# Kernel optimization log

Measured on AMD Instinct MI355X. Metric: run time of the kernel, lower is better.

## Reference

```python
import jax, jax.numpy as jnp
import numpy as np

KH, KW = 3, 3          # kernel_size
SH, SW = 1, 1          # stride
PH, PW = 1, 1          # padding
NCODEBOOKS = 16
SUBVEC = 36            # (64*3*3)/16
K = 16                 # codewords per codebook (4 tree levels)


def _unfold(x):
    """torch.nn.functional.unfold equivalent: (b,c,h,w) -> (b, c*KH*KW, oh, ow),
    feature dim ordered channel-major (c, ki, kj) like torch."""
    b, c, h, w = x.shape
    xp = jnp.pad(x, ((0, 0), (0, 0), (PH, PH), (PW, PW)))
    oh = (h + 2 * PH - KH) // SH + 1
    ow = (w + 2 * PW - KW) // SW + 1
    patches = [xp[:, :, i:i + (oh - 1) * SH + 1:SH, j:j + (ow - 1) * SW + 1:SW]
               for i in range(KH) for j in range(KW)]
    cols = jnp.stack(patches, axis=2)              # (b, c, KH*KW, oh, ow)
    return cols.reshape(b, c * KH * KW, oh, ow)


def setup_inputs() -> dict:
    key = jax.random.key(0)
    k1, k2, k3, k4, k5 = jax.random.split(key, 5)
    return {
        "x": jax.random.normal(k1, (16, 64, 56, 56), dtype=jnp.float32),
        "split_idxs": jax.random.randint(k2, (NCODEBOOKS, 4), 0, SUBVEC, dtype=jnp.int32),
        "split_vals": jax.random.normal(k3, (NCODEBOOKS, 4, K // 2), dtype=jnp.float32),
        "lookup_tables": jax.random.normal(k4, (NCODEBOOKS, K, 64), dtype=jnp.float32),
        "bias": jax.random.normal(k5, (64,), dtype=jnp.float32),
    }


def reference(x, split_idxs, split_vals, lookup_tables, bias):
    b = x.shape[0]
    cols = _unfold(x)                              # (b, d, oh, ow)
    _, d, oh, ow = cols.shape
    # torch: cols.permute(0,2,1).flatten(0,1) with L=oh*ow row-major
    xf = cols.reshape(b, d, oh * ow).transpose(0, 2, 1).reshape(-1, d)  # (n, d)
    n = xf.shape[0]
    xs = xf.reshape(n, NCODEBOOKS, SUBVEC)
    car = jnp.arange(NCODEBOOKS)
    # Hierarchical 4-level threshold encoding (vectorized over all codebooks):
    # at level t, a point in bucket e compares feature split_idxs[c,t] against
    # split_vals[c,t,e]; new bucket = 2*e + (v >= thr)  (matches the serial
    # bucket-list construction: '<' -> left child, '>=' -> right child).
    enc = jnp.zeros((n, NCODEBOOKS), dtype=jnp.int32)
    for t in range(4):
        v = xs[:, car, split_idxs[:, t]]           # (n, NCODEBOOKS)
        thr = split_vals[car[None, :], t, enc]     # (n, NCODEBOOKS)
        enc = 2 * enc + (v >= thr).astype(jnp.int32)
    # LUT gather-sum (equivalent to one_hot(enc) @ lookup_tables[i], summed)
    gathered = lookup_tables[car[None, :], enc]    # (n, NCODEBOOKS, out_ch)
    out = gathered.sum(axis=1) + bias              # (n, out_ch)
    out = out.reshape(b, oh, ow, -1).transpose(0, 3, 1, 2)
    return out
```

## Files before the change

### kernel.cpp

```cpp
#include <hip/hip_runtime.h>
#include <hip/hip_fp16.h>

static constexpr int W56 = 56;
static constexpr int SP  = 56 * 56;
static constexpr int CHN = 64;

__global__ __launch_bounds__(256) void lut_prep(const float* __restrict__ lut,
                                                __half* __restrict__ wlut) {
    const int t = blockIdx.x * 256 + threadIdx.x;
    const int r = t >> 3;
    const int c = (t & 7) ^ (r & 7);
    const float4* src = reinterpret_cast<const float4*>(lut + r * 64 + c * 8);
    const float4 f0 = src[0];
    const float4 f1 = src[1];
    __half2 h[4];
    h[0] = __float22half2_rn(make_float2(f0.x, f0.y));
    h[1] = __float22half2_rn(make_float2(f0.z, f0.w));
    h[2] = __float22half2_rn(make_float2(f1.x, f1.y));
    h[3] = __float22half2_rn(make_float2(f1.z, f1.w));
    *reinterpret_cast<float4*>(wlut + t * 8) = *reinterpret_cast<const float4*>(h);
}

__device__ __forceinline__ void async_copy16(const void* g, void* l) {
    __builtin_amdgcn_global_load_lds(
        (const __attribute__((address_space(1))) void*)g,
        (__attribute__((address_space(3))) void*)l,
        16, 0, 0);
}

__global__ __launch_bounds__(256, 4) void maddness_fused(
    const float*  __restrict__ x,
    const int*    __restrict__ si,
    const float*  __restrict__ sv,
    const __half* __restrict__ wlut,
    const float*  __restrict__ bias,
    float*        __restrict__ out)
{
    __shared__ __half2        lutLds[256 * 32];
    __shared__ unsigned short codes[256];

    const int tid  = threadIdx.x;
    const int part = tid >> 6;
    const int lane = tid & 63;
    const int pu   = __builtin_amdgcn_readfirstlane(part);

    const int p  = blockIdx.x * 64 + lane;
    const int b  = p / SP;
    const int s  = p - b * SP;
    const int y  = s / W56;
    const int xc = s - y * W56;
    const float* __restrict__ xb = x + b * (CHN * SP);

    const int* __restrict__ sip = si + pu * 16;
    float v[4][4];
    #pragma unroll
    for (int c = 0; c < 4; ++c) {
        #pragma unroll
        for (int t = 0; t < 4; ++t) {
            const int cb = pu * 4 + c;
            const int g  = sip[c * 4 + t] + cb * 36;
            const int ch = g / 9;
            const int k9 = g - ch * 9;
            const int ki = k9 / 3;
            const int dy = ki - 1;
            const int dx = (k9 - ki * 3) - 1;
            const int yy = y + dy, xx = xc + dx;
            const bool ok = ((unsigned)yy < (unsigned)W56) & ((unsigned)xx < (unsigned)W56);
            const int yyc = min(max(yy, 0), W56 - 1);
            const int xxc = min(max(xx, 0), W56 - 1);
            const float lv = xb[ch * SP + yyc * W56 + xxc];
            v[c][t] = ok ? lv : 0.0f;
        }
    }

    {
        const char* gsrc = reinterpret_cast<const char*>(wlut) + pu * 8192 + lane * 16;
        char*       ldst = reinterpret_cast<char*>(lutLds) + pu * 8192;
        #pragma unroll
        for (int i = 0; i < 8; ++i)
            async_copy16(gsrc + i * 1024, ldst + i * 1024);
    }

    const float* __restrict__ svp = sv + pu * 128;
    float T0[4], T1[4][2], T2[4][4], T3[4][8];
    #pragma unroll
    for (int c = 0; c < 4; ++c) {
        const int base = c * 32;
        T0[c] = svp[base];
        #pragma unroll
        for (int j = 0; j < 2; ++j) T1[c][j] = svp[base + 8  + j];
        #pragma unroll
        for (int j = 0; j < 4; ++j) T2[c][j] = svp[base + 16 + j];
        #pragma unroll
        for (int j = 0; j < 8; ++j) T3[c][j] = svp[base + 24 + j];
    }

    unsigned code = 0;
    #pragma unroll
    for (int c = 0; c < 4; ++c) {
        const bool b0 = v[c][0] >= T0[c];
        const float t1 = b0 ? T1[c][1] : T1[c][0];
        const bool b1 = v[c][1] >= t1;
        const float s01 = b1 ? T2[c][1] : T2[c][0];
        const float s23 = b1 ? T2[c][3] : T2[c][2];
        const bool b2 = v[c][2] >= (b0 ? s23 : s01);
        const float w0 = b2 ? T3[c][1] : T3[c][0];
        const float w1 = b2 ? T3[c][3] : T3[c][2];
        const float w2 = b2 ? T3[c][5] : T3[c][4];
        const float w3 = b2 ? T3[c][7] : T3[c][6];
        const float z0 = b1 ? w1 : w0;
        const float z1 = b1 ? w3 : w2;
        const bool b3 = v[c][3] >= (b0 ? z1 : z0);
        const int e = ((int)b0 << 3) | ((int)b1 << 2) | ((int)b2 << 1) | (int)b3;
        code |= (unsigned)e << (4 * c);
    }
    codes[part * 64 + lane] = (unsigned short)code;
    __syncthreads();

    const int q = part;
    const unsigned cd0 = codes[lane];
    const unsigned cd1 = codes[64 + lane];
    const unsigned cd2 = codes[128 + lane];
    const unsigned cd3 = codes[192 + lane];

    __half2 acc[8];
    #pragma unroll
    for (int r = 0; r < 8; ++r) acc[r] = __half2{__half(0.0f), __half(0.0f)};

    #pragma unroll
    for (int cb = 0; cb < 16; ++cb) {
        const unsigned cw = (cb < 4) ? cd0 : (cb < 8) ? cd1 : (cb < 12) ? cd2 : cd3;
        const int e   = (int)((cw >> ((cb & 3) * 4)) & 15u);
        const int row = cb * 16 + e;
        const int swz = e & 7;
        const int c0  = (2 * q) ^ swz;
        const int c1  = c0 ^ 1;
        const __half2* __restrict__ base = &lutLds[row * 32];
        const float4 ra = *reinterpret_cast<const float4*>(base + c0 * 4);
        const float4 rb = *reinterpret_cast<const float4*>(base + c1 * 4);
        const __half2* ha = reinterpret_cast<const __half2*>(&ra);
        const __half2* hb = reinterpret_cast<const __half2*>(&rb);
        #pragma unroll
        for (int r = 0; r < 4; ++r) {
            acc[r]     += ha[r];
            acc[4 + r] += hb[r];
        }
    }

    float* __restrict__ op = out + b * (CHN * SP) + (q * 16) * SP + s;
    const float* __restrict__ bq = bias + q * 16;
    #pragma unroll
    for (int r = 0; r < 8; ++r) {
        const float2 f = __half22float2(acc[r]);
        op[(2 * r)     * SP] = f.x + bq[2 * r];
        op[(2 * r + 1) * SP] = f.y + bq[2 * r + 1];
    }
}

extern "C" void kernel_launch(void* const* d_in, const int* in_sizes, int n_in,
                              void* d_out, int out_size, void* d_ws, size_t ws_size,
                              hipStream_t stream) {
    const float* x  = (const float*)d_in[0];
    const int*   si = (const int*)  d_in[1];
    const float* sv = (const float*)d_in[2];
    const float* lt = (const float*)d_in[3];
    const float* bs = (const float*)d_in[4];
    float* o = (float*)d_out;
    __half* wlut = (__half*)d_ws;

    lut_prep<<<dim3(8), dim3(256), 0, stream>>>(lt, wlut);
    maddness_fused<<<dim3(784), dim3(256), 0, stream>>>(x, si, sv, wlut, bs, o);
}
```

Baseline: 77.07 us.

## Process two pixel groups per block to amortize LUT staging

Each block now handles two 64-pixel groups instead of one, halving the grid to 392 blocks. The 32KB LUT copy into LDS is amortized over twice the work, and encoding of the second group overlaps the decode of the first using double-buffered code slots. Launch bounds are relaxed to 2 blocks per CU. The cost is fewer blocks than CUs' worth of parallelism slots (392 blocks on 256 CUs) and higher register pressure.

```diff
diff --git a/kernel.cpp b/kernel.cpp
--- a/kernel.cpp
+++ b/kernel.cpp
@@ -28,7 +28,7 @@
         16, 0, 0);
 }
 
-__global__ __launch_bounds__(256, 4) void maddness_fused(
+__global__ __launch_bounds__(256, 2) void maddness_fused(
     const float*  __restrict__ x,
     const int*    __restrict__ si,
     const float*  __restrict__ sv,
@@ -37,39 +37,47 @@
     float*        __restrict__ out)
 {
     __shared__ __half2        lutLds[256 * 32];
-    __shared__ unsigned short codes[256];
+    __shared__ unsigned short codes[2][256];
 
     const int tid  = threadIdx.x;
     const int part = tid >> 6;
     const int lane = tid & 63;
     const int pu   = __builtin_amdgcn_readfirstlane(part);
 
-    const int p  = blockIdx.x * 64 + lane;
-    const int b  = p / SP;
-    const int s  = p - b * SP;
-    const int y  = s / W56;
-    const int xc = s - y * W56;
-    const float* __restrict__ xb = x + b * (CHN * SP);
-
     const int* __restrict__ sip = si + pu * 16;
-    float v[4][4];
+
+    const int g0 = blockIdx.x * 2;
+    int bb[2], ss[2], yy0[2], xx0[2];
     #pragma unroll
-    for (int c = 0; c < 4; ++c) {
-        #pragma unroll
-        for (int t = 0; t < 4; ++t) {
-            const int cb = pu * 4 + c;
-            const int g  = sip[c * 4 + t] + cb * 36;
-            const int ch = g / 9;
-            const int k9 = g - ch * 9;
-            const int ki = k9 / 3;
-            const int dy = ki - 1;
-            const int dx = (k9 - ki * 3) - 1;
-            const int yy = y + dy, xx = xc + dx;
-            const bool ok = ((unsigned)yy < (unsigned)W56) & ((unsigned)xx < (unsigned)W56);
-            const int yyc = min(max(yy, 0), W56 - 1);
-            const int xxc = min(max(xx, 0), W56 - 1);
-            const float lv = xb[ch * SP + yyc * W56 + xxc];
-            v[c][t] = ok ? lv : 0.0f;
+    for (int g = 0; g < 2; ++g) {
+        const int p = (g0 + g) * 64 + lane;
+        bb[g]  = p / SP;
+        ss[g]  = p - bb[g] * SP;
+        yy0[g] = ss[g] / W56;
+        xx0[g] = ss[g] - yy0[g] * W56;
+    }
+
+    float v0[4][4], v1[4][4];
+    {
+        const float* __restrict__ xb = x + bb[0] * (CHN * SP);
+        #pragma unroll
+        for (int c = 0; c < 4; ++c) {
+            #pragma unroll
+            for (int t = 0; t < 4; ++t) {
+                const int cb = pu * 4 + c;
+                const int g  = sip[c * 4 + t] + cb * 36;
+                const int ch = g / 9;
+                const int k9 = g - ch * 9;
+                const int ki = k9 / 3;
+                const int dy = ki - 1;
+                const int dx = (k9 - ki * 3) - 1;
+                const int yv = yy0[0] + dy, xv = xx0[0] + dx;
+                const bool ok = ((unsigned)yv < (unsigned)W56) & ((unsigned)xv < (unsigned)W56);
+                const int yc = min(max(yv, 0), W56 - 1);
+                const int xc = min(max(xv, 0), W56 - 1);
+                const float lv = xb[ch * SP + yc * W56 + xc];
+                v0[c][t] = ok ? lv : 0.0f;
+            }
         }
     }
 
@@ -79,6 +87,29 @@
         #pragma unroll
         for (int i = 0; i < 8; ++i)
             async_copy16(gsrc + i * 1024, ldst + i * 1024);
+    }
+
+    {
+        const float* __restrict__ xb = x + bb[1] * (CHN * SP);
+        #pragma unroll
+        for (int c = 0; c < 4; ++c) {
+            #pragma unroll
+            for (int t = 0; t < 4; ++t) {
+                const int cb = pu * 4 + c;
+                const int g  = sip[c * 4 + t] + cb * 36;
+                const int ch = g / 9;
+                const int k9 = g - ch * 9;
+                const int ki = k9 / 3;
+                const int dy = ki - 1;
+                const int dx = (k9 - ki * 3) - 1;
+                const int yv = yy0[1] + dy, xv = xx0[1] + dx;
+                const bool ok = ((unsigned)yv < (unsigned)W56) & ((unsigned)xv < (unsigned)W56);
+                const int yc = min(max(yv, 0), W56 - 1);
+                const int xc = min(max(xv, 0), W56 - 1);
+                const float lv = xb[ch * SP + yc * W56 + xc];
+                v1[c][t] = ok ? lv : 0.0f;
+            }
+        }
     }
 
     const float* __restrict__ svp = sv + pu * 128;
@@ -95,66 +126,78 @@
         for (int j = 0; j < 8; ++j) T3[c][j] = svp[base + 24 + j];
     }
 
-    unsigned code = 0;
-    #pragma unroll
-    for (int c = 0; c < 4; ++c) {
-        const bool b0 = v[c][0] >= T0[c];
-        const float t1 = b0 ? T1[c][1] : T1[c][0];
-        const bool b1 = v[c][1] >= t1;
-        const float s01 = b1 ? T2[c][1] : T2[c][0];
-        const float s23 = b1 ? T2[c][3] : T2[c][2];
-        const bool b2 = v[c][2] >= (b0 ? s23 : s01);
-        const float w0 = b2 ? T3[c][1] : T3[c][0];
-        const float w1 = b2 ? T3[c][3] : T3[c][2];
-        const float w2 = b2 ? T3[c][5] : T3[c][4];
-        const float w3 = b2 ? T3[c][7] : T3[c][6];
-        const float z0 = b1 ? w1 : w0;
-        const float z1 = b1 ? w3 : w2;
-        const bool b3 = v[c][3] >= (b0 ? z1 : z0);
-        const int e = ((int)b0 << 3) | ((int)b1 << 2) | ((int)b2 << 1) | (int)b3;
-        code |= (unsigned)e << (4 * c);
-    }
-    codes[part * 64 + lane] = (unsigned short)code;
+    auto encode = [&](const float v[4][4]) -> unsigned {
+        unsigned code = 0;
+        #pragma unroll
+        for (int c = 0; c < 4; ++c) {
+            const bool b0 = v[c][0] >= T0[c];
+            const float t1 = b0 ? T1[c][1] : T1[c][0];
+            const bool b1 = v[c][1] >= t1;
+            const float s01 = b1 ? T2[c][1] : T2[c][0];
+            const float s23 = b1 ? T2[c][3] : T2[c][2];
+            const bool b2 = v[c][2] >= (b0 ? s23 : s01);
+            const float w0 = b2 ? T3[c][1] : T3[c][0];
+            const float w1 = b2 ? T3[c][3] : T3[c][2];
+            const float w2 = b2 ? T3[c][5] : T3[c][4];
+            const float w3 = b2 ? T3[c][7] : T3[c][6];
+            const float z0 = b1 ? w1 : w0;
+            const float z1 = b1 ? w3 : w2;
+            const bool b3 = v[c][3] >= (b0 ? z1 : z0);
+            const int e = ((int)b0 << 3) | ((int)b1 << 2) | ((int)b2 << 1) | (int)b3;
+            code |= (unsigned)e << (4 * c);
+        }
+        return code;
+    };
+
+    const int q = part;
+    auto decode_store = [&](int slot, int gi) {
+        const unsigned cd0 = codes[slot][lane];
+        const unsigned cd1 = codes[slot][64 + lane];
+        const unsigned cd2 = codes[slot][128 + lane];
+        const unsigned cd3 = codes[slot][192 + lane];
+
+        __half2 acc[8];
+        #pragma unroll
+        for (int r = 0; r < 8; ++r) acc[r] = __half2{__half(0.0f), __half(0.0f)};
+
+        #pragma unroll
+        for (int cb = 0; cb < 16; ++cb) {
+            const unsigned cw = (cb < 4) ? cd0 : (cb < 8) ? cd1 : (cb < 12) ? cd2 : cd3;
+            const int e   = (int)((cw >> ((cb & 3) * 4)) & 15u);
+            const int row = cb * 16 + e;
+            const int swz = e & 7;
+            const int c0  = (2 * q) ^ swz;
+            const int c1  = c0 ^ 1;
+            const __half2* __restrict__ base = &lutLds[row * 32];
+            const float4 ra = *reinterpret_cast<const float4*>(base + c0 * 4);
+            const float4 rb = *reinterpret_cast<const float4*>(base + c1 * 4);
+            const __half2* ha = reinterpret_cast<const __half2*>(&ra);
+            const __half2* hb = reinterpret_cast<const __half2*>(&rb);
+            #pragma unroll
+            for (int r = 0; r < 4; ++r) {
+                acc[r]     += ha[r];
+                acc[4 + r] += hb[r];
+            }
+        }
+
+        float* __restrict__ op = out + bb[gi] * (CHN * SP) + (q * 16) * SP + ss[gi];
+        const float* __restrict__ bq = bias + q * 16;
+        #pragma unroll
+        for (int r = 0; r < 8; ++r) {
+            const float2 f = __half22float2(acc[r]);
+            op[(2 * r)     * SP] = f.x + bq[2 * r];
+            op[(2 * r + 1) * SP] = f.y + bq[2 * r + 1];
+        }
+    };
+
+    codes[0][part * 64 + lane] = (unsigned short)encode(v0);
     __syncthreads();
 
-    const int q = part;
-    const unsigned cd0 = codes[lane];
-    const unsigned cd1 = codes[64 + lane];
-    const unsigned cd2 = codes[128 + lane];
-    const unsigned cd3 = codes[192 + lane];
-
-    __half2 acc[8];
-    #pragma unroll
-    for (int r = 0; r < 8; ++r) acc[r] = __half2{__half(0.0f), __half(0.0f)};
-
-    #pragma unroll
-    for (int cb = 0; cb < 16; ++cb) {
-        const unsigned cw = (cb < 4) ? cd0 : (cb < 8) ? cd1 : (cb < 12) ? cd2 : cd3;
-        const int e   = (int)((cw >> ((cb & 3) * 4)) & 15u);
-        const int row = cb * 16 + e;
-        const int swz = e & 7;
-        const int c0  = (2 * q) ^ swz;
-        const int c1  = c0 ^ 1;
-        const __half2* __restrict__ base = &lutLds[row * 32];
-        const float4 ra = *reinterpret_cast<const float4*>(base + c0 * 4);
-        const float4 rb = *reinterpret_cast<const float4*>(base + c1 * 4);
-        const __half2* ha = reinterpret_cast<const __half2*>(&ra);
-        const __half2* hb = reinterpret_cast<const __half2*>(&rb);
-        #pragma unroll
-        for (int r = 0; r < 4; ++r) {
-            acc[r]     += ha[r];
-            acc[4 + r] += hb[r];
-        }
-    }
-
-    float* __restrict__ op = out + b * (CHN * SP) + (q * 16) * SP + s;
-    const float* __restrict__ bq = bias + q * 16;
-    #pragma unroll
-    for (int r = 0; r < 8; ++r) {
-        const float2 f = __half22float2(acc[r]);
-        op[(2 * r)     * SP] = f.x + bq[2 * r];
-        op[(2 * r + 1) * SP] = f.y + bq[2 * r + 1];
-    }
+    codes[1][part * 64 + lane] = (unsigned short)encode(v1);
+    decode_store(0, 0);
+
+    __syncthreads();
+    decode_store(1, 1);
 }
 
 extern "C" void kernel_launch(void* const* d_in, const int* in_sizes, int n_in,
@@ -169,5 +212,5 @@
     __half* wlut = (__half*)d_ws;
 
     lut_prep<<<dim3(8), dim3(256), 0, stream>>>(lt, wlut);
-    maddness_fused<<<dim3(784), dim3(256), 0, stream>>>(x, si, sv, wlut, bs, o);
-}
+    maddness_fused<<<dim3(392), dim3(256), 0, stream>>>(x, si, sv, wlut, bs, o);
+}
```

New measurement: 77.76 us. About the same (+0.9%).
